# Performance work log

Measured on AMD Instinct MI355X. Metric: run time of the kernel, lower is better.

The kernel has to match this reference:

```python
import jax, jax.numpy as jnp
import numpy as np

N, E, H = 50000, 800000, 4
IN_C, HID, OUT = 256, 64, 64
NEG_SLOPE = 0.2   # PyG GATConv default leaky_relu slope
EPS_BN = 1e-5
EPS_SM = 1e-16    # PyG softmax denominator eps


def setup_inputs() -> dict:
    key = jax.random.key(0)
    ks = jax.random.split(key, 16)
    inp = {
        "x": jax.random.normal(ks[0], (N, IN_C), jnp.float32),
        "edge_index": jax.random.randint(ks[1], (2, E), 0, N, jnp.int32),
    }
    dims = [(IN_C, HID), (HID, HID), (HID, OUT)]
    j = 2
    for l, (di, do) in enumerate(dims):
        s = 1.0 / np.sqrt(di)
        inp[f"W{l}"] = jax.random.normal(ks[j], (di, H * do), jnp.float32) * s; j += 1
        inp[f"as{l}"] = jax.random.normal(ks[j], (H, do), jnp.float32) * 0.1; j += 1
        inp[f"ad{l}"] = jax.random.normal(ks[j], (H, do), jnp.float32) * 0.1; j += 1
        inp[f"b{l}"] = jnp.zeros((do,), jnp.float32)
    for l in range(2):  # BN after all but the last conv
        inp[f"g{l}"] = jnp.ones((HID,), jnp.float32)
        inp[f"be{l}"] = jnp.zeros((HID,), jnp.float32)
    return inp


def _gat_layer(x, src, dst, W, a_src, a_dst, bias):
    """PyG GATConv, heads=H, concat=False (mean over heads), add_self_loops already in src/dst."""
    n = x.shape[0]
    C = a_src.shape[1]
    h = (x @ W).reshape(n, H, C)                      # [N,H,C]
    a_l = jnp.einsum('nhc,hc->nh', h, a_src)          # src attention term per node
    a_r = jnp.einsum('nhc,hc->nh', h, a_dst)          # dst attention term per node
    e = jax.nn.leaky_relu(a_l[src] + a_r[dst], NEG_SLOPE)   # [E',H]
    # segment softmax over incoming edges of each dst node
    m = jax.ops.segment_max(e, dst, num_segments=n)
    m = jnp.where(jnp.isfinite(m), m, 0.0)
    p = jnp.exp(e - m[dst])
    den = jax.ops.segment_sum(p, dst, num_segments=n)
    alpha = p / (den[dst] + EPS_SM)                   # [E',H]
    msg = h[src] * alpha[:, :, None]                  # [E',H,C]
    out = jax.ops.segment_sum(msg, dst, num_segments=n)
    return out.mean(axis=1) + bias                    # concat=False -> head mean, then bias


def _bn(x, g, b):
    # BatchNorm1d training-mode statistics (biased variance), eps=1e-5
    mu = x.mean(axis=0)
    var = x.var(axis=0)
    return (x - mu) * jax.lax.rsqrt(var + EPS_BN) * g + b


def reference(x, edge_index, W0, as0, ad0, b0, W1, as1, ad1, b1,
              W2, as2, ad2, b2, g0, be0, g1, be1):
    n = x.shape[0]
    loops = jnp.arange(n, dtype=edge_index.dtype)
    src = jnp.concatenate([edge_index[0], loops])
    dst = jnp.concatenate([edge_index[1], loops])

    h = _gat_layer(x, src, dst, W0, as0, ad0, b0)
    h = jax.nn.relu(_bn(h, g0, be0))                  # dropout: eval mode (identity)
    h = _gat_layer(h, src, dst, W1, as1, ad1, b1)
    h = jax.nn.relu(_bn(h, g1, be1))
    out = _gat_layer(h, src, dst, W2, as2, ad2, b2)
    return out
```

## Files before the change

kernel.cpp:

```cpp
#include <hip/hip_runtime.h>
#include <hip/hip_fp16.h>
#include <math.h>

constexpr float NEG_SLOPE = 0.2f;
constexpr float EPS_BN = 1e-5f;
constexpr float EPS_SM = 1e-16f;

typedef _Float16 half8 __attribute__((ext_vector_type(8)));
typedef float f32x4 __attribute__((ext_vector_type(4)));

__device__ __forceinline__ float lrelu(float x){ return x >= 0.f ? x : NEG_SLOPE * x; }

typedef const __attribute__((address_space(1))) unsigned int* gas_u32;
typedef __attribute__((address_space(3))) unsigned int* las_u32;

__device__ __forceinline__ void llds16(const _Float16* g, _Float16* l){
  __builtin_amdgcn_global_load_lds((gas_u32)(const void*)g, (las_u32)(void*)l, 16, 0, 0);
}

__global__ void k_prep1(const float* __restrict__ x, _Float16* __restrict__ xh, int n8,
                        const int* __restrict__ ei, int E, int* __restrict__ cnt,
                        int* __restrict__ rank,
                        const float* __restrict__ W0, const float* __restrict__ W1,
                        const float* __restrict__ W2, _Float16* __restrict__ Wt0,
                        _Float16* __restrict__ Wtp1, _Float16* __restrict__ Wtp2,
                        const float* __restrict__ as1, const float* __restrict__ ad1,
                        const float* __restrict__ as2, const float* __restrict__ ad2,
                        float* __restrict__ va,
                        float* __restrict__ bn, int* __restrict__ tick){
  int t = blockIdx.x * blockDim.x + threadIdx.x;
  if (t < n8){
    const float4* p = (const float4*)(x + (size_t)t * 8);
    float4 v0 = p[0], v1 = p[1];
    half8 h = {(_Float16)v0.x, (_Float16)v0.y, (_Float16)v0.z, (_Float16)v0.w,
               (_Float16)v1.x, (_Float16)v1.y, (_Float16)v1.z, (_Float16)v1.w};
    *(half8*)(xh + (size_t)t * 8) = h;
  }
  if (t < E) rank[t] = atomicAdd(&cnt[ei[E + t]], 1);
  if (t < 256) bn[t] = 0.f;
  if (t < 4) tick[t] = 0;
  if (t < 65536){
    int c = t & 255, k = t >> 8;
    Wt0[(size_t)c * 256 + k] = (_Float16)W0[(size_t)k * 256 + c];
  } else if (t < 81920){
    int u = t - 65536; int c = u & 63, r = u >> 6;
    Wtp1[(size_t)c * 256 + r] = (_Float16)(0.25f * W1[(size_t)(r & 63) * 256 + (r >> 6) * 64 + c]);
  } else if (t < 98304){
    int u = t - 81920; int c = u & 63, r = u >> 6;
    Wtp2[(size_t)c * 256 + r] = (_Float16)(0.25f * W2[(size_t)(r & 63) * 256 + (r >> 6) * 64 + c]);
  } else if (t < 99328){
    int u = t - 98304;
    int layer = u >> 9;
    int sd = (u >> 8) & 1;
    int u2 = u & 255;
    int c = u2 >> 2, h = u2 & 3;
    const float* Wl = layer ? W2 : W1;
    const float* av = layer ? (sd ? ad2 : as2) : (sd ? ad1 : as1);
    float acc = 0.f;
    #pragma unroll 4
    for (int k = 0; k < 64; k++)
      acc += Wl[(size_t)c * 256 + h * 64 + k] * av[h * 64 + k];
    va[layer * 512 + c * 8 + sd * 4 + h] = acc;
  }
}

__global__ __launch_bounds__(256) void k_bsumscan(const int* __restrict__ cnt, int n, int chunk,
                                                  int* __restrict__ part, int* __restrict__ ptr,
                                                  int* __restrict__ tick){
  __shared__ int s[256];
  __shared__ int amLast;
  int b = blockIdx.x, t = threadIdx.x;
  int lo = b * chunk, hi = min(n, lo + chunk);
  int v = 0;
  for (int i = lo + t; i < hi; i += 256) v += cnt[i] + 1;
  s[t] = v;
  __syncthreads();
  #pragma unroll
  for (int off = 128; off > 0; off >>= 1){
    if (t < off) s[t] += s[t + off];
    __syncthreads();
  }
  if (t == 0) part[b] = s[0];
  __threadfence();
  if (t == 0) amLast = (atomicAdd(tick, 1) == (int)gridDim.x - 1) ? 1 : 0;
  __syncthreads();
  if (amLast){
    int pv = atomicAdd(&part[t], 0);
    s[t] = pv;
    __syncthreads();
    #pragma unroll
    for (int off = 1; off < 256; off <<= 1){
      int u = (t >= off) ? s[t - off] : 0;
      __syncthreads();
      s[t] += u;
      __syncthreads();
    }
    part[t] = s[t] - pv;
    if (t == 255) ptr[n] = s[255];
  }
}

__global__ __launch_bounds__(256) void k_localscan(const int* __restrict__ cnt, const int* __restrict__ part,
                                                   int n, int chunk, int* __restrict__ ptr,
                                                   int* __restrict__ csr_src){
  __shared__ int s[256];
  int b = blockIdx.x, t = threadIdx.x;
  int i = b * chunk + t;
  int c = (t < chunk && i < n) ? cnt[i] : 0;
  int v = (t < chunk && i < n) ? c + 1 : 0;
  s[t] = v;
  __syncthreads();
  #pragma unroll
  for (int off = 1; off < 256; off <<= 1){
    int u = (t >= off) ? s[t - off] : 0;
    __syncthreads();
    s[t] += u;
    __syncthreads();
  }
  if (t < chunk && i < n){
    int ex = part[b] + s[t] - v;
    ptr[i] = ex;
    csr_src[ex + c] = i;
  }
}

template<int LAYER>
__global__ __launch_bounds__(256, 2) void k_gemm(const _Float16* __restrict__ Xh,
    const _Float16* __restrict__ Wt, const float* __restrict__ a_s, const float* __restrict__ a_d,
    __half* __restrict__ hb, float* __restrict__ al, float* __restrict__ ar, int nrows,
    const int* __restrict__ ei, int E, const int* __restrict__ rank,
    const int* __restrict__ rowptr, int* __restrict__ csr_src,
    int gemmBlocks, int N){
  constexpr int K = 256;
  if (LAYER == 0 && (int)blockIdx.x >= gemmBlocks){
    int fb = (int)blockIdx.x - gemmBlocks;
    int xcd = (int)blockIdx.x & 7;
    int grp = fb >> 3;
    int ngrp = ((int)gridDim.x - gemmBlocks) >> 3;
    int nPer = N >> 3;
    int lo = xcd * nPer;
    int hi = (xcd == 7) ? N : lo + nPer;
    int stride = ngrp * 256;
    for (int e = grp * 256 + (int)threadIdx.x; e < E; e += stride){
      int dst = ei[E + e];
      if (dst >= lo && dst < hi)
        csr_src[rowptr[dst] + rank[e]] = ei[e];
    }
    return;
  }
  __shared__ _Float16 Alds[4][129][8];
  __shared__ _Float16 Blds[4][257][8];
  int tid = threadIdx.x;
  int m0 = blockIdx.x * 128;
  int w = tid >> 6, l = tid & 63;
  int lm = l & 15, lq = l >> 4;
  f32x4 acc[8][4] = {};

  for (int k0 = 0; k0 < K; k0 += 32){
    #pragma unroll
    for (int it = 0; it < 2; it++){
      int gr = m0 + it * 64 + l;
      if (gr < nrows)
        llds16(Xh + (size_t)gr * K + k0 + w * 8, &Alds[w][it * 64][0]);
    }
    #pragma unroll
    for (int it = 0; it < 4; it++){
      int col = it * 64 + l;
      llds16(Wt + (size_t)col * K + k0 + w * 8, &Blds[w][it * 64][0]);
    }
    __syncthreads();
    half8 af[8];
    #pragma unroll
    for (int mf = 0; mf < 8; mf++) af[mf] = *(const half8*)&Alds[lq][mf * 16 + lm][0];
    #pragma unroll
    for (int j = 0; j < 4; j++){
      half8 bf = *(const half8*)&Blds[lq][(w * 4 + j) * 16 + lm][0];
      #pragma unroll
      for (int mf = 0; mf < 8; mf++)
        acc[mf][j] = __builtin_amdgcn_mfma_f32_16x16x32_f16(af[mf], bf, acc[mf][j], 0, 0, 0);
    }
    __syncthreads();
  }

  float asv[4], adv[4];
  #pragma unroll
  for (int j = 0; j < 4; j++){
    asv[j] = a_s[w * 64 + j * 16 + lm];
    adv[j] = a_d[w * 64 + j * 16 + lm];
  }
  #pragma unroll
  for (int mf = 0; mf < 8; mf++){
    #pragma unroll
    for (int reg = 0; reg < 4; reg++){
      float sl = acc[mf][0][reg] * asv[0] + acc[mf][1][reg] * asv[1]
               + acc[mf][2][reg] * asv[2] + acc[mf][3][reg] * asv[3];
      float sr = acc[mf][0][reg] * adv[0] + acc[mf][1][reg] * adv[1]
               + acc[mf][2][reg] * adv[2] + acc[mf][3][reg] * adv[3];
      #pragma unroll
      for (int off = 1; off < 16; off <<= 1){
        sl += __shfl_xor(sl, off);
        sr += __shfl_xor(sr, off);
      }
      int row = m0 + mf * 16 + lq * 4 + reg;
      if (lm == 0 && row < nrows){
        al[(size_t)row * 4 + w] = sl;
        ar[(size_t)row * 4 + w] = sr;
      }
      if (row < nrows){
        ushort4 pk;
        pk.x = __half_as_ushort(__float2half(acc[mf][0][reg]));
        pk.y = __half_as_ushort(__float2half(acc[mf][1][reg]));
        pk.z = __half_as_ushort(__float2half(acc[mf][2][reg]));
        pk.w = __half_as_ushort(__float2half(acc[mf][3][reg]));
        *(ushort4*)(hb + (size_t)row * 256 + w * 64 + lm * 4) = pk;
      }
    }
  }
}

#define AGG_STEP(QV, POFF) { \
    int je = j + (POFF) + eh; \
    float w = wbase[je * 4 + hd]; \
    int4 qq = QV; \
    int jn = je + 8; \
    if (jn < deg){ \
      int s = sbase[jn]; \
      QV = *(const int4*)((const char*)hb + (((unsigned)s << 9) + choff)); \
    } \
    const __half2* h2 = (const __half2*)&qq; \
    float2 f0 = __half22float2(h2[0]); \
    float2 f1 = __half22float2(h2[1]); \
    float2 f2 = __half22float2(h2[2]); \
    float2 f3 = __half22float2(h2[3]); \
    a0 = fmaf(f0.x, w, a0); a1 = fmaf(f0.y, w, a1); \
    a2 = fmaf(f1.x, w, a2); a3 = fmaf(f1.y, w, a3); \
    a4 = fmaf(f2.x, w, a4); a5 = fmaf(f2.y, w, a5); \
    a6 = fmaf(f3.x, w, a6); a7 = fmaf(f3.y, w, a7); \
  }

__global__ __launch_bounds__(256, 8) void k_node(const int* __restrict__ ptr,
    const int* __restrict__ csr, const __half* __restrict__ hb,
    const float* __restrict__ al, const float* __restrict__ ar,
    const float* __restrict__ bias, float* __restrict__ out, int N){
  __shared__ float4 wsm[4][64];
  __shared__ int    ssm[4][64];
  int n = (blockIdx.x * blockDim.x + threadIdx.x) >> 6;
  int lane = threadIdx.x & 63;
  int wv = threadIdx.x >> 6;
  if (n >= N) return;
  int beg = ptr[n], end = ptr[n + 1];
  int deg = end - beg;
  float4 arv = *(const float4*)(ar + (size_t)n * 4);

  if (deg <= 64){
    int idx = beg + lane;
    bool act = idx < end;
    int mye = act ? csr[idx] : 0;
    int eh = lane >> 5;
    int hd = (lane >> 3) & 3;
    int c8 = lane & 7;
    unsigned choff = (unsigned)(hd * 128 + c8 * 16);

    float e0 = -1e30f, e1 = -1e30f, e2 = -1e30f, e3 = -1e30f;
    if (act){
      float4 av = *(const float4*)((const char*)al + ((unsigned)mye << 4));
      e0 = lrelu(av.x + arv.x); e1 = lrelu(av.y + arv.y);
      e2 = lrelu(av.z + arv.z); e3 = lrelu(av.w + arv.w);
    }
    int s0 = __shfl(mye, 0 + eh), s1 = __shfl(mye, 2 + eh);
    int s2 = __shfl(mye, 4 + eh), s3 = __shfl(mye, 6 + eh);
    int4 q0 = *(const int4*)((const char*)hb + (((unsigned)s0 << 9) + choff));
    int4 q1 = *(const int4*)((const char*)hb + (((unsigned)s1 << 9) + choff));
    int4 q2 = *(const int4*)((const char*)hb + (((unsigned)s2 << 9) + choff));
    int4 q3 = *(const int4*)((const char*)hb + (((unsigned)s3 << 9) + choff));

    float m0 = e0, m1 = e1, m2 = e2, m3 = e3;
    #pragma unroll
    for (int off = 32; off > 0; off >>= 1){
      m0 = fmaxf(m0, __shfl_xor(m0, off));
      m1 = fmaxf(m1, __shfl_xor(m1, off));
      m2 = fmaxf(m2, __shfl_xor(m2, off));
      m3 = fmaxf(m3, __shfl_xor(m3, off));
    }
    float w0 = __expf(e0 - m0), w1 = __expf(e1 - m1);
    float w2 = __expf(e2 - m2), w3 = __expf(e3 - m3);
    float d0 = w0, d1 = w1, d2 = w2, d3 = w3;
    #pragma unroll
    for (int off = 32; off > 0; off >>= 1){
      d0 += __shfl_xor(d0, off);
      d1 += __shfl_xor(d1, off);
      d2 += __shfl_xor(d2, off);
      d3 += __shfl_xor(d3, off);
    }
    wsm[wv][lane] = make_float4(w0 / (d0 + EPS_SM), w1 / (d1 + EPS_SM),
                                w2 / (d2 + EPS_SM), w3 / (d3 + EPS_SM));
    ssm[wv][lane] = mye;
    __builtin_amdgcn_wave_barrier();

    const float* wbase = (const float*)&wsm[wv][0];
    const int*   sbase = &ssm[wv][0];
    float a0=0.f,a1=0.f,a2=0.f,a3=0.f,a4=0.f,a5=0.f,a6=0.f,a7=0.f;
    for (int j = 0; j < deg; j += 8){
      AGG_STEP(q0, 0)
      AGG_STEP(q1, 2)
      AGG_STEP(q2, 4)
      AGG_STEP(q3, 6)
    }
    #pragma unroll
    for (int off = 32; off >= 8; off >>= 1){
      a0 += __shfl_xor(a0, off); a1 += __shfl_xor(a1, off);
      a2 += __shfl_xor(a2, off); a3 += __shfl_xor(a3, off);
      a4 += __shfl_xor(a4, off); a5 += __shfl_xor(a5, off);
      a6 += __shfl_xor(a6, off); a7 += __shfl_xor(a7, off);
    }
    if (lane < 8){
      float* op = out + (size_t)n * 64 + c8 * 2;
      float2 b0 = *(const float2*)(bias + 0 * 16 + c8 * 2);
      float2 b1 = *(const float2*)(bias + 1 * 16 + c8 * 2);
      float2 b2 = *(const float2*)(bias + 2 * 16 + c8 * 2);
      float2 b3 = *(const float2*)(bias + 3 * 16 + c8 * 2);
      *(float2*)(op + 0)  = make_float2(a0 * 0.25f + b0.x, a4 * 0.25f + b0.y);
      *(float2*)(op + 16) = make_float2(a1 * 0.25f + b1.x, a5 * 0.25f + b1.y);
      *(float2*)(op + 32) = make_float2(a2 * 0.25f + b2.x, a6 * 0.25f + b2.y);
      *(float2*)(op + 48) = make_float2(a3 * 0.25f + b3.x, a7 * 0.25f + b3.y);
    }
  } else {
    int hd = lane >> 4;
    int t = lane & 15;
    const __half* hbase = hb + hd * 64 + t * 4;
    float ax = 0.f, ay = 0.f, az = 0.f, aw = 0.f;
    float m0 = -1e30f, m1 = -1e30f, m2 = -1e30f, m3 = -1e30f;
    for (int i = beg + lane; i < end; i += 64){
      int s = csr[i];
      float4 av = *(const float4*)(al + (size_t)s * 4);
      m0 = fmaxf(m0, lrelu(av.x + arv.x));
      m1 = fmaxf(m1, lrelu(av.y + arv.y));
      m2 = fmaxf(m2, lrelu(av.z + arv.z));
      m3 = fmaxf(m3, lrelu(av.w + arv.w));
    }
    #pragma unroll
    for (int off = 32; off > 0; off >>= 1){
      m0 = fmaxf(m0, __shfl_xor(m0, off));
      m1 = fmaxf(m1, __shfl_xor(m1, off));
      m2 = fmaxf(m2, __shfl_xor(m2, off));
      m3 = fmaxf(m3, __shfl_xor(m3, off));
    }
    float d0 = 0.f, d1 = 0.f, d2 = 0.f, d3 = 0.f;
    for (int i = beg + lane; i < end; i += 64){
      int s = csr[i];
      float4 av = *(const float4*)(al + (size_t)s * 4);
      d0 += __expf(lrelu(av.x + arv.x) - m0);
      d1 += __expf(lrelu(av.y + arv.y) - m1);
      d2 += __expf(lrelu(av.z + arv.z) - m2);
      d3 += __expf(lrelu(av.w + arv.w) - m3);
    }
    #pragma unroll
    for (int off = 32; off > 0; off >>= 1){
      d0 += __shfl_xor(d0, off);
      d1 += __shfl_xor(d1, off);
      d2 += __shfl_xor(d2, off);
      d3 += __shfl_xor(d3, off);
    }
    float i0 = 1.f / (d0 + EPS_SM), i1 = 1.f / (d1 + EPS_SM);
    float i2 = 1.f / (d2 + EPS_SM), i3 = 1.f / (d3 + EPS_SM);
    float arh = hd == 0 ? arv.x : hd == 1 ? arv.y : hd == 2 ? arv.z : arv.w;
    float mh  = hd == 0 ? m0 : hd == 1 ? m1 : hd == 2 ? m2 : m3;
    float ih  = hd == 0 ? i0 : hd == 1 ? i1 : hd == 2 ? i2 : i3;
    for (int i = beg; i < end; i++){
      int s = csr[i];
      float w = __expf(lrelu(al[(size_t)s * 4 + hd] + arh) - mh) * ih;
      ushort4 u = *(const ushort4*)(hbase + (size_t)s * 256);
      ax = fmaf(__half2float(__ushort_as_half(u.x)), w, ax);
      ay = fmaf(__half2float(__ushort_as_half(u.y)), w, ay);
      az = fmaf(__half2float(__ushort_as_half(u.z)), w, az);
      aw = fmaf(__half2float(__ushort_as_half(u.w)), w, aw);
    }
    #pragma unroll
    for (int off = 16; off <= 32; off <<= 1){
      ax += __shfl_xor(ax, off);
      ay += __shfl_xor(ay, off);
      az += __shfl_xor(az, off);
      aw += __shfl_xor(aw, off);
    }
    if (lane < 16){
      float* op = out + (size_t)n * 64;
      op[t]      = ax * 0.25f + bias[t];
      op[16 + t] = ay * 0.25f + bias[16 + t];
      op[32 + t] = az * 0.25f + bias[32 + t];
      op[48 + t] = aw * 0.25f + bias[48 + t];
    }
  }
}

__global__ __launch_bounds__(256) void k_attn(const float* __restrict__ bufA,
    const float* __restrict__ scale, const float* __restrict__ shift,
    const float* __restrict__ va,
    _Float16* __restrict__ yh, float* __restrict__ al, float* __restrict__ ar, int N){
  int n = (blockIdx.x * 256 + threadIdx.x) >> 4;
  int t = threadIdx.x & 15;
  if (n >= N) return;
  float4 v  = *(const float4*)(bufA + (size_t)n * 64 + t * 4);
  float4 sc = *(const float4*)(scale + t * 4);
  float4 sh = *(const float4*)(shift + t * 4);
  float y0 = fmaxf(fmaf(v.x, sc.x, sh.x), 0.f);
  float y1 = fmaxf(fmaf(v.y, sc.y, sh.y), 0.f);
  float y2 = fmaxf(fmaf(v.z, sc.z, sh.z), 0.f);
  float y3 = fmaxf(fmaf(v.w, sc.w, sh.w), 0.f);
  ushort4 pk;
  pk.x = __half_as_ushort(__float2half(y0));
  pk.y = __half_as_ushort(__float2half(y1));
  pk.z = __half_as_ushort(__float2half(y2));
  pk.w = __half_as_ushort(__float2half(y3));
  *(ushort4*)(yh + (size_t)n * 64 + t * 4) = pk;

  float p0=0,p1=0,p2=0,p3=0,p4=0,p5=0,p6=0,p7=0;
  #define ATT_ACC(YV, J) { \
    const float4 a = *(const float4*)(va + (t * 4 + (J)) * 8); \
    const float4 b = *(const float4*)(va + (t * 4 + (J)) * 8 + 4); \
    p0 = fmaf(YV, a.x, p0); p1 = fmaf(YV, a.y, p1); \
    p2 = fmaf(YV, a.z, p2); p3 = fmaf(YV, a.w, p3); \
    p4 = fmaf(YV, b.x, p4); p5 = fmaf(YV, b.y, p5); \
    p6 = fmaf(YV, b.z, p6); p7 = fmaf(YV, b.w, p7); }
  ATT_ACC(y0, 0) ATT_ACC(y1, 1) ATT_ACC(y2, 2) ATT_ACC(y3, 3)
  #undef ATT_ACC
  #pragma unroll
  for (int off = 1; off < 16; off <<= 1){
    p0 += __shfl_xor(p0, off); p1 += __shfl_xor(p1, off);
    p2 += __shfl_xor(p2, off); p3 += __shfl_xor(p3, off);
    p4 += __shfl_xor(p4, off); p5 += __shfl_xor(p5, off);
    p6 += __shfl_xor(p6, off); p7 += __shfl_xor(p7, off);
  }
  if (t == 0){
    *(float4*)(al + (size_t)n * 4) = make_float4(p0, p1, p2, p3);
    *(float4*)(ar + (size_t)n * 4) = make_float4(p4, p5, p6, p7);
  }
}

#define AGG_FMA(Q, W4) { \
    union { uint2 u; __half2 h[2]; } _u; _u.u = (Q); \
    float2 _fa = __half22float2(_u.h[0]); \
    float2 _fb = __half22float2(_u.h[1]); \
    a0.x = fmaf(_fa.x, (W4).x, a0.x); a0.y = fmaf(_fa.y, (W4).x, a0.y); \
    a0.z = fmaf(_fb.x, (W4).x, a0.z); a0.w = fmaf(_fb.y, (W4).x, a0.w); \
    a1.x = fmaf(_fa.x, (W4).y, a1.x); a1.y = fmaf(_fa.y, (W4).y, a1.y); \
    a1.z = fmaf(_fb.x, (W4).y, a1.z); a1.w = fmaf(_fb.y, (W4).y, a1.w); \
    a2.x = fmaf(_fa.x, (W4).z, a2.x); a2.y = fmaf(_fa.y, (W4).z, a2.y); \
    a2.z = fmaf(_fb.x, (W4).z, a2.z); a2.w = fmaf(_fb.y, (W4).z, a2.w); \
    a3.x = fmaf(_fa.x, (W4).w, a3.x); a3.y = fmaf(_fa.y, (W4).w, a3.y); \
    a3.z = fmaf(_fb.x, (W4).w, a3.z); a3.w = fmaf(_fb.y, (W4).w, a3.w); \
  }
#define RED2(V) { V += __shfl_xor(V, 16); V += __shfl_xor(V, 32); }

__global__ __launch_bounds__(256, 8) void k_agg(const int* __restrict__ ptr,
    const int* __restrict__ csr, const _Float16* __restrict__ yh,
    const float* __restrict__ al, const float* __restrict__ ar,
    __half* __restrict__ aggh, int N){
  __shared__ float4 wsm[4][64];
  __shared__ int    ssm[4][64];
  int n = (blockIdx.x * blockDim.x + threadIdx.x) >> 6;
  int lane = threadIdx.x & 63;
  int wv = threadIdx.x >> 6;
  if (n >= N) return;
  int beg = ptr[n], end = ptr[n + 1];
  int deg = end - beg;
  float4 arv = *(const float4*)(ar + (size_t)n * 4);
  int eh = lane >> 4;
  int t  = lane & 15;
  float4 a0 = {0,0,0,0}, a1 = {0,0,0,0}, a2 = {0,0,0,0}, a3 = {0,0,0,0};

  if (deg <= 64){
    int idx = beg + lane;
    bool act = idx < end;
    int mye = act ? csr[idx] : 0;
    float e0 = -1e30f, e1 = -1e30f, e2 = -1e30f, e3 = -1e30f;
    if (act){
      float4 av = *(const float4*)((const char*)al + ((unsigned)mye << 4));
      e0 = lrelu(av.x + arv.x); e1 = lrelu(av.y + arv.y);
      e2 = lrelu(av.z + arv.z); e3 = lrelu(av.w + arv.w);
    }
    int sA = __shfl(mye, eh);
    int sB = __shfl(mye, 4 + eh);
    uint2 qA = *(const uint2*)((const char*)yh + (((unsigned)sA) << 7) + t * 8);
    uint2 qB = *(const uint2*)((const char*)yh + (((unsigned)sB) << 7) + t * 8);

    float m0 = e0, m1 = e1, m2 = e2, m3 = e3;
    #pragma unroll
    for (int off = 32; off > 0; off >>= 1){
      m0 = fmaxf(m0, __shfl_xor(m0, off));
      m1 = fmaxf(m1, __shfl_xor(m1, off));
      m2 = fmaxf(m2, __shfl_xor(m2, off));
      m3 = fmaxf(m3, __shfl_xor(m3, off));
    }
    float w0 = __expf(e0 - m0), w1 = __expf(e1 - m1);
    float w2 = __expf(e2 - m2), w3 = __expf(e3 - m3);
    float d0 = w0, d1 = w1, d2 = w2, d3 = w3;
    #pragma unroll
    for (int off = 32; off > 0; off >>= 1){
      d0 += __shfl_xor(d0, off);
      d1 += __shfl_xor(d1, off);
      d2 += __shfl_xor(d2, off);
      d3 += __shfl_xor(d3, off);
    }
    wsm[wv][lane] = make_float4(w0 / (d0 + EPS_SM), w1 / (d1 + EPS_SM),
                                w2 / (d2 + EPS_SM), w3 / (d3 + EPS_SM));
    ssm[wv][lane] = mye;
    __builtin_amdgcn_wave_barrier();

    for (int j = 0; j < deg; j += 8){
      uint2 cur = qA;
      if (j + 8 < deg){
        int s2 = ssm[wv][j + 8 + eh];
        qA = *(const uint2*)((const char*)yh + (((unsigned)s2) << 7) + t * 8);
      }
      float4 w4 = wsm[wv][j + eh];
      AGG_FMA(cur, w4)
      uint2 curB = qB;
      if (j + 12 < deg){
        int s3 = ssm[wv][j + 12 + eh];
        qB = *(const uint2*)((const char*)yh + (((unsigned)s3) << 7) + t * 8);
      }
      float4 w4b = wsm[wv][j + 4 + eh];
      AGG_FMA(curB, w4b)
    }
  } else {
    float m0 = -1e30f, m1 = -1e30f, m2 = -1e30f, m3 = -1e30f;
    for (int i = beg + lane; i < end; i += 64){
      int s = csr[i];
      float4 av = *(const float4*)(al + (size_t)s * 4);
      m0 = fmaxf(m0, lrelu(av.x + arv.x));
      m1 = fmaxf(m1, lrelu(av.y + arv.y));
      m2 = fmaxf(m2, lrelu(av.z + arv.z));
      m3 = fmaxf(m3, lrelu(av.w + arv.w));
    }
    #pragma unroll
    for (int off = 32; off > 0; off >>= 1){
      m0 = fmaxf(m0, __shfl_xor(m0, off));
      m1 = fmaxf(m1, __shfl_xor(m1, off));
      m2 = fmaxf(m2, __shfl_xor(m2, off));
      m3 = fmaxf(m3, __shfl_xor(m3, off));
    }
    float d0 = 0.f, d1 = 0.f, d2 = 0.f, d3 = 0.f;
    for (int i = beg + lane; i < end; i += 64){
      int s = csr[i];
      float4 av = *(const float4*)(al + (size_t)s * 4);
      d0 += __expf(lrelu(av.x + arv.x) - m0);
      d1 += __expf(lrelu(av.y + arv.y) - m1);
      d2 += __expf(lrelu(av.z + arv.z) - m2);
      d3 += __expf(lrelu(av.w + arv.w) - m3);
    }
    #pragma unroll
    for (int off = 32; off > 0; off >>= 1){
      d0 += __shfl_xor(d0, off);
      d1 += __shfl_xor(d1, off);
      d2 += __shfl_xor(d2, off);
      d3 += __shfl_xor(d3, off);
    }
    float i0 = 1.f / (d0 + EPS_SM), i1 = 1.f / (d1 + EPS_SM);
    float i2 = 1.f / (d2 + EPS_SM), i3 = 1.f / (d3 + EPS_SM);
    for (int i = beg; i < end; i += 4){
      int ie = i + eh;
      float w0 = 0.f, w1 = 0.f, w2 = 0.f, w3 = 0.f;
      int s = 0;
      if (ie < end){
        s = csr[ie];
        float4 av = *(const float4*)(al + (size_t)s * 4);
        w0 = __expf(lrelu(av.x + arv.x) - m0) * i0;
        w1 = __expf(lrelu(av.y + arv.y) - m1) * i1;
        w2 = __expf(lrelu(av.z + arv.z) - m2) * i2;
        w3 = __expf(lrelu(av.w + arv.w) - m3) * i3;
      }
      uint2 q = *(const uint2*)((const char*)yh + (((unsigned)s) << 7) + t * 8);
      float4 w4 = make_float4(w0, w1, w2, w3);
      AGG_FMA(q, w4)
    }
  }

  RED2(a0.x) RED2(a0.y) RED2(a0.z) RED2(a0.w)
  RED2(a1.x) RED2(a1.y) RED2(a1.z) RED2(a1.w)
  RED2(a2.x) RED2(a2.y) RED2(a2.z) RED2(a2.w)
  RED2(a3.x) RED2(a3.y) RED2(a3.z) RED2(a3.w)
  if (eh == 0){
    char* base = (char*)aggh + ((size_t)n << 9) + t * 8;
    ushort4 pk;
    pk.x = __half_as_ushort(__float2half(a0.x));
    pk.y = __half_as_ushort(__float2half(a0.y));
    pk.z = __half_as_ushort(__float2half(a0.z));
    pk.w = __half_as_ushort(__float2half(a0.w));
    *(ushort4*)(base + 0)   = pk;
    pk.x = __half_as_ushort(__float2half(a1.x));
    pk.y = __half_as_ushort(__float2half(a1.y));
    pk.z = __half_as_ushort(__float2half(a1.z));
    pk.w = __half_as_ushort(__float2half(a1.w));
    *(ushort4*)(base + 128) = pk;
    pk.x = __half_as_ushort(__float2half(a2.x));
    pk.y = __half_as_ushort(__float2half(a2.y));
    pk.z = __half_as_ushort(__float2half(a2.z));
    pk.w = __half_as_ushort(__float2half(a2.w));
    *(ushort4*)(base + 256) = pk;
    pk.x = __half_as_ushort(__float2half(a3.x));
    pk.y = __half_as_ushort(__float2half(a3.y));
    pk.z = __half_as_ushort(__float2half(a3.z));
    pk.w = __half_as_ushort(__float2half(a3.w));
    *(ushort4*)(base + 384) = pk;
  }
}

__global__ __launch_bounds__(256, 2) void k_gemmp(const _Float16* __restrict__ A,
    const _Float16* __restrict__ Bt,
    const float* __restrict__ bias, float* __restrict__ out, int nrows){
  __shared__ _Float16 Alds[4][257][8];
  __shared__ _Float16 Blds[4][65][8];
  int tid = threadIdx.x;
  int m0 = blockIdx.x * 256;
  int w = tid >> 6, l = tid & 63;
  int lm = l & 15, lq = l >> 4;
  f32x4 acc[4][4] = {};
  for (int k0 = 0; k0 < 256; k0 += 32){
    #pragma unroll
    for (int it = 0; it < 4; it++){
      int gr = m0 + it * 64 + l;
      if (gr < nrows)
        llds16(A + (size_t)gr * 256 + k0 + w * 8, &Alds[w][it * 64][0]);
    }
    llds16(Bt + (size_t)l * 256 + k0 + w * 8, &Blds[w][0][0]);
    __syncthreads();
    half8 af[4];
    #pragma unroll
    for (int mf = 0; mf < 4; mf++) af[mf] = *(const half8*)&Alds[lq][w * 64 + mf * 16 + lm][0];
    #pragma unroll
    for (int j = 0; j < 4; j++){
      half8 bf = *(const half8*)&Blds[lq][j * 16 + lm][0];
      #pragma unroll
      for (int mf = 0; mf < 4; mf++)
        acc[mf][j] = __builtin_amdgcn_mfma_f32_16x16x32_f16(af[mf], bf, acc[mf][j], 0, 0, 0);
    }
    __syncthreads();
  }
  float bv[4];
  #pragma unroll
  for (int j = 0; j < 4; j++) bv[j] = bias[j * 16 + lm];
  #pragma unroll
  for (int mf = 0; mf < 4; mf++){
    #pragma unroll
    for (int reg = 0; reg < 4; reg++){
      int row = m0 + w * 64 + mf * 16 + lq * 4 + reg;
      if (row < nrows){
        #pragma unroll
        for (int j = 0; j < 4; j++)
          out[(size_t)row * 64 + j * 16 + lm] = acc[mf][j][reg] + bv[j];
      }
    }
  }
}

__global__ __launch_bounds__(256) void k_bnstats(const float* __restrict__ x, int N,
                                                 float* __restrict__ gsum, float* __restrict__ gsq,
                                                 int* __restrict__ tick,
                                                 const float* __restrict__ g, const float* __restrict__ be,
                                                 float* __restrict__ scale, float* __restrict__ shift){
  int c = threadIdx.x & 63;
  int rg = threadIdx.x >> 6;
  float s = 0.f, q = 0.f;
  for (int r = blockIdx.x * 4 + rg; r < N; r += gridDim.x * 4){
    float v = x[(size_t)r * 64 + c];
    s += v; q += v * v;
  }
  __shared__ float ls[4][64], lq[4][64];
  __shared__ int amLast;
  ls[rg][c] = s; lq[rg][c] = q;
  __syncthreads();
  if (rg == 0){
    s = ls[0][c] + ls[1][c] + ls[2][c] + ls[3][c];
    q = lq[0][c] + lq[1][c] + lq[2][c] + lq[3][c];
    atomicAdd(&gsum[c], s);
    atomicAdd(&gsq[c], q);
  }
  __threadfence();
  if (threadIdx.x == 0)
    amLast = (atomicAdd(tick, 1) == (int)gridDim.x - 1) ? 1 : 0;
  __syncthreads();
  if (amLast && threadIdx.x < 64){
    float gs = atomicAdd(&gsum[c], 0.f);
    float gq = atomicAdd(&gsq[c], 0.f);
    float m = gs / (float)N;
    float v = gq / (float)N - m * m;
    float sc = g[c] * rsqrtf(v + EPS_BN);
    scale[c] = sc;
    shift[c] = be[c] - m * sc;
  }
}

extern "C" void kernel_launch(void* const* d_in, const int* in_sizes, int n_in,
                              void* d_out, int out_size, void* d_ws, size_t ws_size,
                              hipStream_t stream){
  const float* x  = (const float*)d_in[0];
  const int*   ei = (const int*)d_in[1];
  const float* W[3]  = {(const float*)d_in[2], (const float*)d_in[6],  (const float*)d_in[10]};
  const float* AS[3] = {(const float*)d_in[3], (const float*)d_in[7],  (const float*)d_in[11]};
  const float* AD[3] = {(const float*)d_in[4], (const float*)d_in[8],  (const float*)d_in[12]};
  const float* BI[3] = {(const float*)d_in[5], (const float*)d_in[9],  (const float*)d_in[13]};
  const float* G[2]  = {(const float*)d_in[14], (const float*)d_in[16]};
  const float* BE[2] = {(const float*)d_in[15], (const float*)d_in[17]};
  const int N = in_sizes[0] / 256;
  const int E = in_sizes[1] / 2;
  const int EN = E + N;

  char* wsb = (char*)d_ws;
  size_t off = 0;
  auto alloc = [&](size_t bytes) -> char* {
    char* p = wsb + off;
    off = (off + bytes + 255) & ~(size_t)255;
    return p;
  };
  int* cnt      = (int*)alloc((size_t)N * 4);
  int* rowptr   = (int*)alloc((size_t)(N + 1) * 4);
  int* part     = (int*)alloc(256 * 4);
  int* rank     = (int*)alloc((size_t)E * 4);
  int* csr      = (int*)alloc((size_t)EN * 4);
  _Float16* xh  = (_Float16*)alloc((size_t)N * 256 * 2);
  _Float16* Wt0 = (_Float16*)alloc((size_t)256 * 256 * 2);
  _Float16* Wtp1= (_Float16*)alloc((size_t)64 * 256 * 2);
  _Float16* Wtp2= (_Float16*)alloc((size_t)64 * 256 * 2);
  __half* hb    = (__half*)alloc((size_t)N * 256 * 2);
  float* al     = (float*)alloc((size_t)N * 4 * 4);
  float* ar     = (float*)alloc((size_t)N * 4 * 4);
  float* bufA   = (float*)alloc((size_t)N * 64 * 4);
  _Float16* yh  = (_Float16*)alloc((size_t)N * 64 * 2);
  float* va     = (float*)alloc(1024 * 4);
  float* bn     = (float*)alloc(256 * 4);
  int*   tick   = (int*)alloc(4 * 4);
  float* murs   = (float*)alloc(128 * 4);

  const int chunk = (N + 255) / 256;
  const int n8 = N * 32;
  const int nodeGrid = (N + 3) / 4;
  const int attnGrid = (N + 15) / 16;
  const int gemmpGrid = (N + 255) / 256;

  hipMemsetAsync(cnt, 0, (size_t)N * 4, stream);
  k_prep1<<<(n8 + 255) / 256, 256, 0, stream>>>(x, xh, n8, ei, E, cnt, rank,
                                                W[0], W[1], W[2], Wt0, Wtp1, Wtp2,
                                                AS[1], AD[1], AS[2], AD[2], va, bn, tick);
  k_bsumscan<<<256, 256, 0, stream>>>(cnt, N, chunk, part, rowptr, tick + 2);
  k_localscan<<<256, 256, 0, stream>>>(cnt, part, N, chunk, rowptr, csr);

  int gemmGrid = (N + 127) / 128;
  const int FILLB = 1024;
  k_gemm<0><<<gemmGrid + FILLB, 256, 0, stream>>>(xh, Wt0, AS[0], AD[0], hb, al, ar, N,
                                                  ei, E, rank, rowptr, csr, gemmGrid, N);
  k_node<<<nodeGrid, 256, 0, stream>>>(rowptr, csr, hb, al, ar, BI[0], bufA, N);
  k_bnstats<<<256, 256, 0, stream>>>(bufA, N, bn, bn + 64, tick, G[0], BE[0], murs, murs + 64);
  k_attn<<<attnGrid, 256, 0, stream>>>(bufA, murs, murs + 64, va, yh, al, ar, N);
  k_agg<<<nodeGrid, 256, 0, stream>>>(rowptr, csr, yh, al, ar, hb, N);
  k_gemmp<<<gemmpGrid, 256, 0, stream>>>((const _Float16*)hb, Wtp1, BI[1], bufA, N);
  k_bnstats<<<256, 256, 0, stream>>>(bufA, N, bn + 128, bn + 192, tick + 1, G[1], BE[1], murs, murs + 64);
  k_attn<<<attnGrid, 256, 0, stream>>>(bufA, murs, murs + 64, va + 512, yh, al, ar, N);
  k_agg<<<nodeGrid, 256, 0, stream>>>(rowptr, csr, yh, al, ar, hb, N);
  k_gemmp<<<gemmpGrid, 256, 0, stream>>>((const _Float16*)hb, Wtp2, BI[2], (float*)d_out, N);
}
```

Measured before the change: 525.2 us.

## Process two nodes per wavefront in aggregation when both degrees fit in 32

Each wavefront of k_agg now handles two consecutive destination nodes, one per 32-lane half, when both have at most 32 incoming edges. The softmax reductions shrink to 32 lanes and the final cross-group reduction needs only one shuffle step. This targets lane waste, since the average degree is about 17, so most of a 64-lane wave sat idle. Nodes with higher degree fall back to the old per-node path run sequentially in the same wave, which adds branch and serialization cost for those waves.

```diff
diff --git a/kernel.cpp b/kernel.cpp
--- a/kernel.cpp
+++ b/kernel.cpp
@@ -449,7 +449,31 @@
     a3.x = fmaf(_fa.x, (W4).w, a3.x); a3.y = fmaf(_fa.y, (W4).w, a3.y); \
     a3.z = fmaf(_fb.x, (W4).w, a3.z); a3.w = fmaf(_fb.y, (W4).w, a3.w); \
   }
-#define RED2(V) { V += __shfl_xor(V, 16); V += __shfl_xor(V, 32); }
+
+#define AGG_WRITE(n, t) { \
+    char* base = (char*)aggh + ((size_t)(n) << 9) + (t) * 8; \
+    ushort4 pk; \
+    pk.x = __half_as_ushort(__float2half(a0.x)); \
+    pk.y = __half_as_ushort(__float2half(a0.y)); \
+    pk.z = __half_as_ushort(__float2half(a0.z)); \
+    pk.w = __half_as_ushort(__float2half(a0.w)); \
+    *(ushort4*)(base + 0)   = pk; \
+    pk.x = __half_as_ushort(__float2half(a1.x)); \
+    pk.y = __half_as_ushort(__float2half(a1.y)); \
+    pk.z = __half_as_ushort(__float2half(a1.z)); \
+    pk.w = __half_as_ushort(__float2half(a1.w)); \
+    *(ushort4*)(base + 128) = pk; \
+    pk.x = __half_as_ushort(__float2half(a2.x)); \
+    pk.y = __half_as_ushort(__float2half(a2.y)); \
+    pk.z = __half_as_ushort(__float2half(a2.z)); \
+    pk.w = __half_as_ushort(__float2half(a2.w)); \
+    *(ushort4*)(base + 256) = pk; \
+    pk.x = __half_as_ushort(__float2half(a3.x)); \
+    pk.y = __half_as_ushort(__float2half(a3.y)); \
+    pk.z = __half_as_ushort(__float2half(a3.z)); \
+    pk.w = __half_as_ushort(__float2half(a3.w)); \
+    *(ushort4*)(base + 384) = pk; \
+  }
 
 __global__ __launch_bounds__(256, 8) void k_agg(const int* __restrict__ ptr,
     const int* __restrict__ csr, const _Float16* __restrict__ yh,
@@ -457,35 +481,44 @@
     __half* __restrict__ aggh, int N){
   __shared__ float4 wsm[4][64];
   __shared__ int    ssm[4][64];
-  int n = (blockIdx.x * blockDim.x + threadIdx.x) >> 6;
   int lane = threadIdx.x & 63;
   int wv = threadIdx.x >> 6;
-  if (n >= N) return;
-  int beg = ptr[n], end = ptr[n + 1];
-  int deg = end - beg;
-  float4 arv = *(const float4*)(ar + (size_t)n * 4);
-  int eh = lane >> 4;
-  int t  = lane & 15;
-  float4 a0 = {0,0,0,0}, a1 = {0,0,0,0}, a2 = {0,0,0,0}, a3 = {0,0,0,0};
-
-  if (deg <= 64){
-    int idx = beg + lane;
-    bool act = idx < end;
-    int mye = act ? csr[idx] : 0;
+  int base = (blockIdx.x * 4 + wv) * 2;
+  if (base >= N) return;
+
+  int begA = ptr[base];
+  int endA = ptr[base + 1];
+  int degA = endA - begA;
+  bool dual = (base + 1 < N);
+  int endB = dual ? ptr[base + 2] : endA;
+  int degB = endB - endA;
+
+  if (dual && degA <= 32 && degB <= 32){
+    int h2 = lane >> 5;
+    int l32 = lane & 31;
+    int es = (lane >> 4) & 1;
+    int t = lane & 15;
+    int n = base + h2;
+    int beg = h2 ? endA : begA;
+    int deg = h2 ? degB : degA;
+    float4 arv = *(const float4*)(ar + (size_t)n * 4);
+
+    bool act = l32 < deg;
+    int mye = act ? csr[beg + l32] : 0;
     float e0 = -1e30f, e1 = -1e30f, e2 = -1e30f, e3 = -1e30f;
     if (act){
       float4 av = *(const float4*)((const char*)al + ((unsigned)mye << 4));
       e0 = lrelu(av.x + arv.x); e1 = lrelu(av.y + arv.y);
       e2 = lrelu(av.z + arv.z); e3 = lrelu(av.w + arv.w);
     }
-    int sA = __shfl(mye, eh);
-    int sB = __shfl(mye, 4 + eh);
+    int sA = __shfl(mye, h2 * 32 + es);
+    int sB = __shfl(mye, h2 * 32 + 2 + es);
     uint2 qA = *(const uint2*)((const char*)yh + (((unsigned)sA) << 7) + t * 8);
     uint2 qB = *(const uint2*)((const char*)yh + (((unsigned)sB) << 7) + t * 8);
 
     float m0 = e0, m1 = e1, m2 = e2, m3 = e3;
     #pragma unroll
-    for (int off = 32; off > 0; off >>= 1){
+    for (int off = 16; off > 0; off >>= 1){
       m0 = fmaxf(m0, __shfl_xor(m0, off));
       m1 = fmaxf(m1, __shfl_xor(m1, off));
       m2 = fmaxf(m2, __shfl_xor(m2, off));
@@ -495,7 +528,7 @@
     float w2 = __expf(e2 - m2), w3 = __expf(e3 - m3);
     float d0 = w0, d1 = w1, d2 = w2, d3 = w3;
     #pragma unroll
-    for (int off = 32; off > 0; off >>= 1){
+    for (int off = 16; off > 0; off >>= 1){
       d0 += __shfl_xor(d0, off);
       d1 += __shfl_xor(d1, off);
       d2 += __shfl_xor(d2, off);
@@ -506,102 +539,159 @@
     ssm[wv][lane] = mye;
     __builtin_amdgcn_wave_barrier();
 
-    for (int j = 0; j < deg; j += 8){
+    float4 a0 = {0,0,0,0}, a1 = {0,0,0,0}, a2 = {0,0,0,0}, a3 = {0,0,0,0};
+    int lbase = h2 * 32;
+    for (int j = 0; j < deg; j += 4){
       uint2 cur = qA;
-      if (j + 8 < deg){
-        int s2 = ssm[wv][j + 8 + eh];
+      if (j + 4 < deg){
+        int s2 = ssm[wv][lbase + j + 4 + es];
         qA = *(const uint2*)((const char*)yh + (((unsigned)s2) << 7) + t * 8);
       }
-      float4 w4 = wsm[wv][j + eh];
+      float4 w4 = wsm[wv][lbase + j + es];
       AGG_FMA(cur, w4)
       uint2 curB = qB;
-      if (j + 12 < deg){
-        int s3 = ssm[wv][j + 12 + eh];
+      if (j + 6 < deg){
+        int s3 = ssm[wv][lbase + j + 6 + es];
         qB = *(const uint2*)((const char*)yh + (((unsigned)s3) << 7) + t * 8);
       }
-      float4 w4b = wsm[wv][j + 4 + eh];
+      float4 w4b = wsm[wv][lbase + j + 2 + es];
       AGG_FMA(curB, w4b)
     }
-  } else {
-    float m0 = -1e30f, m1 = -1e30f, m2 = -1e30f, m3 = -1e30f;
-    for (int i = beg + lane; i < end; i += 64){
-      int s = csr[i];
-      float4 av = *(const float4*)(al + (size_t)s * 4);
-      m0 = fmaxf(m0, lrelu(av.x + arv.x));
-      m1 = fmaxf(m1, lrelu(av.y + arv.y));
-      m2 = fmaxf(m2, lrelu(av.z + arv.z));
-      m3 = fmaxf(m3, lrelu(av.w + arv.w));
-    }
-    #pragma unroll
-    for (int off = 32; off > 0; off >>= 1){
-      m0 = fmaxf(m0, __shfl_xor(m0, off));
-      m1 = fmaxf(m1, __shfl_xor(m1, off));
-      m2 = fmaxf(m2, __shfl_xor(m2, off));
-      m3 = fmaxf(m3, __shfl_xor(m3, off));
-    }
-    float d0 = 0.f, d1 = 0.f, d2 = 0.f, d3 = 0.f;
-    for (int i = beg + lane; i < end; i += 64){
-      int s = csr[i];
-      float4 av = *(const float4*)(al + (size_t)s * 4);
-      d0 += __expf(lrelu(av.x + arv.x) - m0);
-      d1 += __expf(lrelu(av.y + arv.y) - m1);
-      d2 += __expf(lrelu(av.z + arv.z) - m2);
-      d3 += __expf(lrelu(av.w + arv.w) - m3);
-    }
-    #pragma unroll
-    for (int off = 32; off > 0; off >>= 1){
-      d0 += __shfl_xor(d0, off);
-      d1 += __shfl_xor(d1, off);
-      d2 += __shfl_xor(d2, off);
-      d3 += __shfl_xor(d3, off);
-    }
-    float i0 = 1.f / (d0 + EPS_SM), i1 = 1.f / (d1 + EPS_SM);
-    float i2 = 1.f / (d2 + EPS_SM), i3 = 1.f / (d3 + EPS_SM);
-    for (int i = beg; i < end; i += 4){
-      int ie = i + eh;
-      float w0 = 0.f, w1 = 0.f, w2 = 0.f, w3 = 0.f;
-      int s = 0;
-      if (ie < end){
-        s = csr[ie];
+    #define R16(V) { V += __shfl_xor(V, 16); }
+    R16(a0.x) R16(a0.y) R16(a0.z) R16(a0.w)
+    R16(a1.x) R16(a1.y) R16(a1.z) R16(a1.w)
+    R16(a2.x) R16(a2.y) R16(a2.z) R16(a2.w)
+    R16(a3.x) R16(a3.y) R16(a3.z) R16(a3.w)
+    #undef R16
+    if (es == 0) AGG_WRITE(n, t)
+    return;
+  }
+
+  int nEnd = dual ? base + 2 : base + 1;
+  for (int n = base; n < nEnd; n++){
+    int beg = ptr[n], end = ptr[n + 1];
+    int deg = end - beg;
+    float4 arv = *(const float4*)(ar + (size_t)n * 4);
+    int eh = lane >> 4;
+    int t  = lane & 15;
+    float4 a0 = {0,0,0,0}, a1 = {0,0,0,0}, a2 = {0,0,0,0}, a3 = {0,0,0,0};
+
+    if (deg <= 64){
+      int idx = beg + lane;
+      bool act = idx < end;
+      int mye = act ? csr[idx] : 0;
+      float e0 = -1e30f, e1 = -1e30f, e2 = -1e30f, e3 = -1e30f;
+      if (act){
+        float4 av = *(const float4*)((const char*)al + ((unsigned)mye << 4));
+        e0 = lrelu(av.x + arv.x); e1 = lrelu(av.y + arv.y);
+        e2 = lrelu(av.z + arv.z); e3 = lrelu(av.w + arv.w);
+      }
+      int sA = __shfl(mye, eh);
+      int sB = __shfl(mye, 4 + eh);
+      uint2 qA = *(const uint2*)((const char*)yh + (((unsigned)sA) << 7) + t * 8);
+      uint2 qB = *(const uint2*)((const char*)yh + (((unsigned)sB) << 7) + t * 8);
+
+      float m0 = e0, m1 = e1, m2 = e2, m3 = e3;
+      #pragma unroll
+      for (int off = 32; off > 0; off >>= 1){
+        m0 = fmaxf(m0, __shfl_xor(m0, off));
+        m1 = fmaxf(m1, __shfl_xor(m1, off));
+        m2 = fmaxf(m2, __shfl_xor(m2, off));
+        m3 = fmaxf(m3, __shfl_xor(m3, off));
+      }
+      float w0 = __expf(e0 - m0), w1 = __expf(e1 - m1);
+      float w2 = __expf(e2 - m2), w3 = __expf(e3 - m3);
+      float d0 = w0, d1 = w1, d2 = w2, d3 = w3;
+      #pragma unroll
+      for (int off = 32; off > 0; off >>= 1){
+        d0 += __shfl_xor(d0, off);
+        d1 += __shfl_xor(d1, off);
+        d2 += __shfl_xor(d2, off);
+        d3 += __shfl_xor(d3, off);
+      }
+      wsm[wv][lane] = make_float4(w0 / (d0 + EPS_SM), w1 / (d1 + EPS_SM),
+                                  w2 / (d2 + EPS_SM), w3 / (d3 + EPS_SM));
+      ssm[wv][lane] = mye;
+      __builtin_amdgcn_wave_barrier();
+
+      for (int j = 0; j < deg; j += 8){
+        uint2 cur = qA;
+        if (j + 8 < deg){
+          int s2 = ssm[wv][j + 8 + eh];
+          qA = *(const uint2*)((const char*)yh + (((unsigned)s2) << 7) + t * 8);
+        }
+        float4 w4 = wsm[wv][j + eh];
+        AGG_FMA(cur, w4)
+        uint2 curB = qB;
+        if (j + 12 < deg){
+          int s3 = ssm[wv][j + 12 + eh];
+          qB = *(const uint2*)((const char*)yh + (((unsigned)s3) << 7) + t * 8);
+        }
+        float4 w4b = wsm[wv][j + 4 + eh];
+        AGG_FMA(curB, w4b)
+      }
+      __builtin_amdgcn_wave_barrier();
+    } else {
+      float m0 = -1e30f, m1 = -1e30f, m2 = -1e30f, m3 = -1e30f;
+      for (int i = beg + lane; i < end; i += 64){
+        int s = csr[i];
         float4 av = *(const float4*)(al + (size_t)s * 4);
-        w0 = __expf(lrelu(av.x + arv.x) - m0) * i0;
-        w1 = __expf(lrelu(av.y + arv.y) - m1) * i1;
-        w2 = __expf(lrelu(av.z + arv.z) - m2) * i2;
-        w3 = __expf(lrelu(av.w + arv.w) - m3) * i3;
-      }
-      uint2 q = *(const uint2*)((const char*)yh + (((unsigned)s) << 7) + t * 8);
-      float4 w4 = make_float4(w0, w1, w2, w3);
-      AGG_FMA(q, w4)
-    }
-  }
-
-  RED2(a0.x) RED2(a0.y) RED2(a0.z) RED2(a0.w)
-  RED2(a1.x) RED2(a1.y) RED2(a1.z) RED2(a1.w)
-  RED2(a2.x) RED2(a2.y) RED2(a2.z) RED2(a2.w)
-  RED2(a3.x) RED2(a3.y) RED2(a3.z) RED2(a3.w)
-  if (eh == 0){
-    char* base = (char*)aggh + ((size_t)n << 9) + t * 8;
-    ushort4 pk;
-    pk.x = __half_as_ushort(__float2half(a0.x));
-    pk.y = __half_as_ushort(__float2half(a0.y));
-    pk.z = __half_as_ushort(__float2half(a0.z));
-    pk.w = __half_as_ushort(__float2half(a0.w));
-    *(ushort4*)(base + 0)   = pk;
-    pk.x = __half_as_ushort(__float2half(a1.x));
-    pk.y = __half_as_ushort(__float2half(a1.y));
-    pk.z = __half_as_ushort(__float2half(a1.z));
-    pk.w = __half_as_ushort(__float2half(a1.w));
-    *(ushort4*)(base + 128) = pk;
-    pk.x = __half_as_ushort(__float2half(a2.x));
-    pk.y = __half_as_ushort(__float2half(a2.y));
-    pk.z = __half_as_ushort(__float2half(a2.z));
-    pk.w = __half_as_ushort(__float2half(a2.w));
-    *(ushort4*)(base + 256) = pk;
-    pk.x = __half_as_ushort(__float2half(a3.x));
-    pk.y = __half_as_ushort(__float2half(a3.y));
-    pk.z = __half_as_ushort(__float2half(a3.z));
-    pk.w = __half_as_ushort(__float2half(a3.w));
-    *(ushort4*)(base + 384) = pk;
+        m0 = fmaxf(m0, lrelu(av.x + arv.x));
+        m1 = fmaxf(m1, lrelu(av.y + arv.y));
+        m2 = fmaxf(m2, lrelu(av.z + arv.z));
+        m3 = fmaxf(m3, lrelu(av.w + arv.w));
+      }
+      #pragma unroll
+      for (int off = 32; off > 0; off >>= 1){
+        m0 = fmaxf(m0, __shfl_xor(m0, off));
+        m1 = fmaxf(m1, __shfl_xor(m1, off));
+        m2 = fmaxf(m2, __shfl_xor(m2, off));
+        m3 = fmaxf(m3, __shfl_xor(m3, off));
+      }
+      float d0 = 0.f, d1 = 0.f, d2 = 0.f, d3 = 0.f;
+      for (int i = beg + lane; i < end; i += 64){
+        int s = csr[i];
+        float4 av = *(const float4*)(al + (size_t)s * 4);
+        d0 += __expf(lrelu(av.x + arv.x) - m0);
+        d1 += __expf(lrelu(av.y + arv.y) - m1);
+        d2 += __expf(lrelu(av.z + arv.z) - m2);
+        d3 += __expf(lrelu(av.w + arv.w) - m3);
+      }
+      #pragma unroll
+      for (int off = 32; off > 0; off >>= 1){
+        d0 += __shfl_xor(d0, off);
+        d1 += __shfl_xor(d1, off);
+        d2 += __shfl_xor(d2, off);
+        d3 += __shfl_xor(d3, off);
+      }
+      float i0 = 1.f / (d0 + EPS_SM), i1 = 1.f / (d1 + EPS_SM);
+      float i2 = 1.f / (d2 + EPS_SM), i3 = 1.f / (d3 + EPS_SM);
+      for (int i = beg; i < end; i += 4){
+        int ie = i + eh;
+        float w0 = 0.f, w1 = 0.f, w2 = 0.f, w3 = 0.f;
+        int s = 0;
+        if (ie < end){
+          s = csr[ie];
+          float4 av = *(const float4*)(al + (size_t)s * 4);
+          w0 = __expf(lrelu(av.x + arv.x) - m0) * i0;
+          w1 = __expf(lrelu(av.y + arv.y) - m1) * i1;
+          w2 = __expf(lrelu(av.z + arv.z) - m2) * i2;
+          w3 = __expf(lrelu(av.w + arv.w) - m3) * i3;
+        }
+        uint2 q = *(const uint2*)((const char*)yh + (((unsigned)s) << 7) + t * 8);
+        float4 w4 = make_float4(w0, w1, w2, w3);
+        AGG_FMA(q, w4)
+      }
+    }
+
+    #define RED2(V) { V += __shfl_xor(V, 16); V += __shfl_xor(V, 32); }
+    RED2(a0.x) RED2(a0.y) RED2(a0.z) RED2(a0.w)
+    RED2(a1.x) RED2(a1.y) RED2(a1.z) RED2(a1.w)
+    RED2(a2.x) RED2(a2.y) RED2(a2.z) RED2(a2.w)
+    RED2(a3.x) RED2(a3.y) RED2(a3.z) RED2(a3.w)
+    #undef RED2
+    if (eh == 0) AGG_WRITE(n, t)
+    __builtin_amdgcn_wave_barrier();
   }
 }
 
@@ -734,6 +824,7 @@
   const int chunk = (N + 255) / 256;
   const int n8 = N * 32;
   const int nodeGrid = (N + 3) / 4;
+  const int aggGrid = (N + 7) / 8;
   const int attnGrid = (N + 15) / 16;
   const int gemmpGrid = (N + 255) / 256;
 
@@ -751,10 +842,10 @@
   k_node<<<nodeGrid, 256, 0, stream>>>(rowptr, csr, hb, al, ar, BI[0], bufA, N);
   k_bnstats<<<256, 256, 0, stream>>>(bufA, N, bn, bn + 64, tick, G[0], BE[0], murs, murs + 64);
   k_attn<<<attnGrid, 256, 0, stream>>>(bufA, murs, murs + 64, va, yh, al, ar, N);
-  k_agg<<<nodeGrid, 256, 0, stream>>>(rowptr, csr, yh, al, ar, hb, N);
+  k_agg<<<aggGrid, 256, 0, stream>>>(rowptr, csr, yh, al, ar, hb, N);
   k_gemmp<<<gemmpGrid, 256, 0, stream>>>((const _Float16*)hb, Wtp1, BI[1], bufA, N);
   k_bnstats<<<256, 256, 0, stream>>>(bufA, N, bn + 128, bn + 192, tick + 1, G[1], BE[1], murs, murs + 64);
   k_attn<<<attnGrid, 256, 0, stream>>>(bufA, murs, murs + 64, va + 512, yh, al, ar, N);
-  k_agg<<<nodeGrid, 256, 0, stream>>>(rowptr, csr, yh, al, ar, hb, N);
+  k_agg<<<aggGrid, 256, 0, stream>>>(rowptr, csr, yh, al, ar, hb, N);
   k_gemmp<<<gemmpGrid, 256, 0, stream>>>((const _Float16*)hb, Wtp2, BI[2], (float*)d_out, N);
 }
```

After: 483.0 us. 8.0% less time.
